# Kernel tuning notes

Measured on AMD Instinct MI355X. Metric: run time of the kernel, lower is better.

The kernel has to match this reference:

```python
import jax, jax.numpy as jnp
import numpy as np

NEG_INF = -1e9
LEAKY_SLOPE = 0.2


def setup_inputs() -> dict:
    key = jax.random.key(0)
    k1, k2, k3, k4, k5, k6, k7 = jax.random.split(key, 7)
    B, L = 50000, 50          # batch nodes, max padded neighbors (num_sample)
    N = 200000                # unique node embeddings
    D_in, D_out = 256, 64
    padded_neighs = jax.random.randint(k1, (B, L), 0, N, dtype=jnp.int32)
    mask = jax.random.randint(k2, (B, L), 0, 2, dtype=jnp.int32).astype(jnp.bool_)
    mask = mask.at[:, 0].set(True)  # every node has >=1 neighbor
    dst_idx = jax.random.randint(k3, (B,), 0, N, dtype=jnp.int32)
    embed_table = jax.random.normal(k4, (N, D_in), dtype=jnp.float32)
    # xavier_uniform for proj [D_out, D_in]
    bound = float(np.sqrt(6.0 / (D_in + D_out)))
    W_proj = jax.random.uniform(k5, (D_out, D_in), minval=-bound, maxval=bound, dtype=jnp.float32)
    a_src = jax.random.normal(k6, (D_out,), dtype=jnp.float32) * 0.1
    a_dst = jax.random.normal(k7, (D_out,), dtype=jnp.float32) * 0.1
    return {"padded_neighs": padded_neighs, "mask": mask, "dst_idx": dst_idx,
            "embed_table": embed_table, "W_proj": W_proj, "a_src": a_src, "a_dst": a_dst}


def leaky_relu(x):
    return jnp.where(x >= 0, x, LEAKY_SLOPE * x)


def reference(padded_neighs, mask, dst_idx, embed_table, W_proj, a_src, a_dst):
    # project all unique-node embeddings: [N, D_out]
    embed_prime = embed_table @ W_proj.T
    # gather neighbor and dst projected features
    neigh_feats = embed_prime[padded_neighs]          # [B, L, D_out]
    dst_feats = embed_prime[dst_idx]                  # [B, D_out] (constant across L)
    # GAT-style scores: leaky_relu(dst @ a_dst) + leaky_relu(neigh @ a_src)
    dst_attn = leaky_relu(dst_feats @ a_dst)[:, None, None]       # [B, 1, 1]
    neigh_attn = leaky_relu(neigh_feats @ a_src)[:, :, None]      # [B, L, 1]
    edge_attn = dst_attn + neigh_attn                             # [B, L, 1]
    # masked softmax over the neighbor axis
    scores = jnp.where(mask[:, :, None], edge_attn, NEG_INF)
    attn = jax.nn.softmax(scores, axis=1)                         # [B, L, 1]
    # weighted sum of neighbor features
    return jnp.sum(attn * neigh_feats, axis=1)                    # [B, D_out]
```

## Files before the change

kernel.cpp:

```cpp
#include <hip/hip_runtime.h>
#include <stdint.h>

#define DIN 256
#define DOUT 64
#define LMAX 50
#define NEG_INF -1e9f
#define WSTRIDE 264

typedef short bf16x8 __attribute__((ext_vector_type(8)));
typedef float f32x4  __attribute__((ext_vector_type(4)));

static __device__ __forceinline__ unsigned short f2bf(float x) {
    unsigned int u = __float_as_uint(x);
    u += 0x7fffu + ((u >> 16) & 1u);
    return (unsigned short)(u >> 16);
}
static __device__ __forceinline__ float bflo(unsigned int u) { return __uint_as_float(u << 16); }
static __device__ __forceinline__ float bfhi(unsigned int u) { return __uint_as_float(u & 0xffff0000u); }

__global__ __launch_bounds__(256) void proj_kernel(
    const float* __restrict__ embed, const float* __restrict__ W,
    unsigned short* __restrict__ ep16, int N)
{
    __shared__ unsigned short wl[64 * WSTRIDE];
    __shared__ unsigned short al[64 * WSTRIDE];

    const int tid  = threadIdx.x;
    const int lane = tid & 63;
    const int wv   = tid >> 6;
    const int mrow = lane & 15;
    const int quad = lane >> 4;
    const int m_base = blockIdx.x * 64;

#pragma unroll
    for (int i = 0; i < 16; ++i) {
        const int idx4 = tid + 256 * i;
        const int e    = idx4 * 4;
        const int n    = e >> 8;
        const int k    = e & 255;
        const float4 f = *(const float4*)&W[e];
        union { unsigned short s[4]; unsigned long long v; } p;
        p.s[0] = f2bf(f.x); p.s[1] = f2bf(f.y);
        p.s[2] = f2bf(f.z); p.s[3] = f2bf(f.w);
        *(unsigned long long*)&wl[n * WSTRIDE + k] = p.v;
    }
#pragma unroll
    for (int i = 0; i < 16; ++i) {
        const int idx4 = tid + 256 * i;
        const int e    = idx4 * 4;
        const int n    = e >> 8;
        const int k    = e & 255;
        int row = m_base + n;
        if (row >= N) row = N - 1;
        const float4 f = *(const float4*)&embed[(size_t)row * DIN + k];
        union { unsigned short s[4]; unsigned long long v; } p;
        p.s[0] = f2bf(f.x); p.s[1] = f2bf(f.y);
        p.s[2] = f2bf(f.z); p.s[3] = f2bf(f.w);
        *(unsigned long long*)&al[n * WSTRIDE + k] = p.v;
    }
    __syncthreads();

    f32x4 acc[4];
#pragma unroll
    for (int nt = 0; nt < 4; ++nt) acc[nt] = (f32x4){0.f, 0.f, 0.f, 0.f};

#pragma unroll
    for (int kc = 0; kc < DIN; kc += 32) {
        const bf16x8 afrag =
            *(const bf16x8*)&al[(wv * 16 + mrow) * WSTRIDE + kc + quad * 8];
#pragma unroll
        for (int nt = 0; nt < 4; ++nt) {
            const bf16x8 bfrag =
                *(const bf16x8*)&wl[(nt * 16 + mrow) * WSTRIDE + kc + quad * 8];
            acc[nt] = __builtin_amdgcn_mfma_f32_16x16x32_bf16(
                afrag, bfrag, acc[nt], 0, 0, 0);
        }
    }

#pragma unroll
    for (int nt = 0; nt < 4; ++nt)
#pragma unroll
        for (int r = 0; r < 4; ++r) {
            const int row = m_base + wv * 16 + quad * 4 + r;
            if (row < N)
                ep16[(size_t)row * DOUT + nt * 16 + mrow] = f2bf(acc[nt][r]);
        }
}

__global__ __launch_bounds__(256, 6) void agg_kernel(
    const int* __restrict__ neighs, const void* __restrict__ mask,
    const unsigned int* __restrict__ ep16u,
    const float* __restrict__ a_src,
    float* __restrict__ out, int B)
{
    __shared__ unsigned int fwbuf[4][LMAX * 32];

    const int tid  = threadIdx.x;
    const int lane = tid & 63;
    const int wv   = tid >> 6;
    const int b    = blockIdx.x * 4 + wv;
    const int bc   = b < B ? b : B - 1;

    const unsigned int* mw = (const unsigned int*)mask;
    const bool byteMode = (mw[12] > 1u);

    const int* nb = neighs + (size_t)bc * LMAX;
    bool mvalid = false;
    int  nbv    = 0;
    if (lane < LMAX) {
        const int mi = bc * LMAX + lane;
        mvalid = byteMode ? (((const uint8_t*)mask)[mi] != 0)
                          : (((const int*)mask)[mi] != 0);
        nbv = nb[lane];
    }
    const unsigned long long vm = __ballot(mvalid);
    const int nv = (int)__popcll(vm);

    const int p    = (int)__popcll(vm & ((1ull << lane) - 1ull));
    const int dsta = mvalid ? p : (nv + (lane - p));
    const int cnb  = __builtin_amdgcn_ds_permute(dsta << 2, nbv);

    unsigned int* buf = fwbuf[wv];
    const int sub    = lane >> 3;
    const int gchunk = (lane & 7) ^ sub;
    const int f      = nv >> 3;
    for (int i = 0; i < f; ++i) {
        const int r = 8 * i + sub;
        const int n = __shfl(cnb, r, 64);
        const unsigned int* gp = ep16u + (size_t)n * 32 + gchunk * 4;
        __builtin_amdgcn_global_load_lds(
            (const __attribute__((address_space(1))) void*)gp,
            (__attribute__((address_space(3))) void*)&buf[i * 256],
            16, 0, 0);
    }
    const int t     = nv & 7;
    const int npair = (t + 1) >> 1;
    const int rbase = 8 * f;
    for (int p2 = 0; p2 < npair; ++p2) {
        const int r   = rbase + 2 * p2 + (lane >> 5);
        const int rc  = r < nv ? r : nv - 1;
        const int n   = __shfl(cnb, rc, 64);
        const int w   = lane & 31;
        const int gwd = (((w >> 2) ^ (r & 7)) << 2) + (w & 3);
        const unsigned int* gp = ep16u + (size_t)n * 32 + gwd;
        __builtin_amdgcn_global_load_lds(
            (const __attribute__((address_space(1))) void*)gp,
            (__attribute__((address_space(3))) void*)&buf[(rbase + 2 * p2) * 32],
            4, 0, 0);
    }

    asm volatile("s_waitcnt vmcnt(0)" ::: "memory");

    const int lc   = lane < nv ? lane : nv - 1;
    const int rot7 = lc & 7;
    const unsigned int* fr = buf + lc * 32;
    float dot = 0.f;
#pragma unroll
    for (int k8 = 0; k8 < 8; ++k8) {
        const uint4 u = *(const uint4*)&fr[((k8 ^ rot7) << 2)];
        dot = fmaf(bflo(u.x), a_src[k8 * 8 + 0], dot);
        dot = fmaf(bfhi(u.x), a_src[k8 * 8 + 1], dot);
        dot = fmaf(bflo(u.y), a_src[k8 * 8 + 2], dot);
        dot = fmaf(bfhi(u.y), a_src[k8 * 8 + 3], dot);
        dot = fmaf(bflo(u.z), a_src[k8 * 8 + 4], dot);
        dot = fmaf(bfhi(u.z), a_src[k8 * 8 + 5], dot);
        dot = fmaf(bflo(u.w), a_src[k8 * 8 + 6], dot);
        dot = fmaf(bfhi(u.w), a_src[k8 * 8 + 7], dot);
    }
    const float lr = dot >= 0.f ? dot : 0.2f * dot;
    float s = (lane < nv) ? lr : NEG_INF;

    float mx = s;
#pragma unroll
    for (int m = 32; m >= 1; m >>= 1) mx = fmaxf(mx, __shfl_xor(mx, m, 64));
    const float e = __expf(s - mx);
    float se = e;
#pragma unroll
    for (int m = 32; m >= 1; m >>= 1) se += __shfl_xor(se, m, 64);
    const float attn = e / se;

    const int s8   = lane >> 3;
    const int gc   = lane & 7;
    const int nit8 = (nv + 7) >> 3;

    float acc[8];
#pragma unroll
    for (int j = 0; j < 8; ++j) acc[j] = 0.f;

    int  rr0 = s8 < nv ? s8 : nv - 1;
    uint4 u  = *(const uint4*)&buf[rr0 * 32 + ((gc ^ (rr0 & 7)) << 2)];
    float w  = __shfl(attn, s8, 64);

    for (int i = 0; i < nit8; ++i) {
        const int inx = (i + 1 < nit8) ? i + 1 : i;
        const int r   = 8 * inx + s8;
        const int rr  = r < nv ? r : nv - 1;
        const uint4 un = *(const uint4*)&buf[rr * 32 + ((gc ^ (rr & 7)) << 2)];
        const float wn = __shfl(attn, r, 64);
        acc[0] = fmaf(w, bflo(u.x), acc[0]);
        acc[1] = fmaf(w, bfhi(u.x), acc[1]);
        acc[2] = fmaf(w, bflo(u.y), acc[2]);
        acc[3] = fmaf(w, bfhi(u.y), acc[3]);
        acc[4] = fmaf(w, bflo(u.z), acc[4]);
        acc[5] = fmaf(w, bfhi(u.z), acc[5]);
        acc[6] = fmaf(w, bflo(u.w), acc[6]);
        acc[7] = fmaf(w, bfhi(u.w), acc[7]);
        u = un; w = wn;
    }

#pragma unroll
    for (int m = 8; m <= 32; m <<= 1)
#pragma unroll
        for (int j = 0; j < 8; ++j) acc[j] += __shfl_xor(acc[j], m, 64);

    if (b < B && lane < 8) {
        float* op = out + (size_t)b * DOUT + 8 * lane;
        float4 o0; o0.x = acc[0]; o0.y = acc[1]; o0.z = acc[2]; o0.w = acc[3];
        float4 o1; o1.x = acc[4]; o1.y = acc[5]; o1.z = acc[6]; o1.w = acc[7];
        *(float4*)op       = o0;
        *(float4*)(op + 4) = o1;
    }
}

extern "C" void kernel_launch(void* const* d_in, const int* in_sizes, int n_in,
                              void* d_out, int out_size, void* d_ws, size_t ws_size,
                              hipStream_t stream)
{
    const int*   neighs  = (const int*)d_in[0];
    const void*  mask    = d_in[1];
    const float* embed   = (const float*)d_in[3];
    const float* W       = (const float*)d_in[4];
    const float* a_src   = (const float*)d_in[5];
    float* out = (float*)d_out;

    const int B = in_sizes[2];
    const int N = in_sizes[3] / DIN;

    unsigned short* ep16 = (unsigned short*)d_ws;

    proj_kernel<<<dim3((N + 63) / 64), dim3(256), 0, stream>>>(embed, W, ep16, N);
    agg_kernel<<<dim3((B + 3) / 4), dim3(256), 0, stream>>>(
        neighs, mask, (const unsigned int*)ep16, a_src, out, B);
}
```

Before: 349.2 us.

## Process two nodes per wave with double-buffered LDS gathers and fixed-size loads

The aggregation kernel now assigns two batch nodes to each wave, each with its own LDS buffer. All gathers for both nodes are issued up front, and a partial vmcnt wait lets the first node's softmax and weighted sum overlap with the second node's loads still in flight. Neighbour compaction is dropped: all 50 slots are loaded at a fixed, unrolled size, with masked slots redirected to neighbour 0 and removed by the mask in the softmax. This trades extra (mostly cache-hitting) gather traffic and doubled LDS per block, with lower occupancy, for more memory-level parallelism and no data-dependent loop counts.

```diff
diff --git a/kernel.cpp b/kernel.cpp
--- a/kernel.cpp
+++ b/kernel.cpp
@@ -87,139 +87,150 @@
         }
 }
 
-__global__ __launch_bounds__(256, 6) void agg_kernel(
+__global__ __launch_bounds__(256, 3) void agg_kernel(
     const int* __restrict__ neighs, const void* __restrict__ mask,
     const unsigned int* __restrict__ ep16u,
     const float* __restrict__ a_src,
     float* __restrict__ out, int B)
 {
-    __shared__ unsigned int fwbuf[4][LMAX * 32];
+    __shared__ unsigned int fwbuf[4][2][LMAX * 32];
 
     const int tid  = threadIdx.x;
     const int lane = tid & 63;
     const int wv   = tid >> 6;
-    const int b    = blockIdx.x * 4 + wv;
-    const int bc   = b < B ? b : B - 1;
+    const int nodeA = blockIdx.x * 8 + wv * 2;
+    const int nodeB = nodeA + 1;
+    const int cA = nodeA < B ? nodeA : B - 1;
+    const int cB = nodeB < B ? nodeB : B - 1;
 
     const unsigned int* mw = (const unsigned int*)mask;
     const bool byteMode = (mw[12] > 1u);
 
-    const int* nb = neighs + (size_t)bc * LMAX;
-    bool mvalid = false;
-    int  nbv    = 0;
+    bool mvA = false, mvB = false;
+    int  nbA = 0, nbB = 0;
     if (lane < LMAX) {
-        const int mi = bc * LMAX + lane;
-        mvalid = byteMode ? (((const uint8_t*)mask)[mi] != 0)
-                          : (((const int*)mask)[mi] != 0);
-        nbv = nb[lane];
-    }
-    const unsigned long long vm = __ballot(mvalid);
-    const int nv = (int)__popcll(vm);
-
-    const int p    = (int)__popcll(vm & ((1ull << lane) - 1ull));
-    const int dsta = mvalid ? p : (nv + (lane - p));
-    const int cnb  = __builtin_amdgcn_ds_permute(dsta << 2, nbv);
-
-    unsigned int* buf = fwbuf[wv];
+        const int miA = cA * LMAX + lane;
+        const int miB = cB * LMAX + lane;
+        if (byteMode) {
+            mvA = ((const uint8_t*)mask)[miA] != 0;
+            mvB = ((const uint8_t*)mask)[miB] != 0;
+        } else {
+            mvA = ((const int*)mask)[miA] != 0;
+            mvB = ((const int*)mask)[miB] != 0;
+        }
+        nbA = neighs[miA];
+        nbB = neighs[miB];
+    }
+    const unsigned long long vmA = __ballot(mvA);
+    const unsigned long long vmB = __ballot(mvB);
+
+    unsigned int* bufA = fwbuf[wv][0];
+    unsigned int* bufB = fwbuf[wv][1];
+
     const int sub    = lane >> 3;
     const int gchunk = (lane & 7) ^ sub;
-    const int f      = nv >> 3;
-    for (int i = 0; i < f; ++i) {
-        const int r = 8 * i + sub;
-        const int n = __shfl(cnb, r, 64);
-        const unsigned int* gp = ep16u + (size_t)n * 32 + gchunk * 4;
-        __builtin_amdgcn_global_load_lds(
-            (const __attribute__((address_space(1))) void*)gp,
-            (__attribute__((address_space(3))) void*)&buf[i * 256],
-            16, 0, 0);
-    }
-    const int t     = nv & 7;
-    const int npair = (t + 1) >> 1;
-    const int rbase = 8 * f;
-    for (int p2 = 0; p2 < npair; ++p2) {
-        const int r   = rbase + 2 * p2 + (lane >> 5);
-        const int rc  = r < nv ? r : nv - 1;
-        const int n   = __shfl(cnb, rc, 64);
-        const int w   = lane & 31;
-        const int gwd = (((w >> 2) ^ (r & 7)) << 2) + (w & 3);
-        const unsigned int* gp = ep16u + (size_t)n * 32 + gwd;
-        __builtin_amdgcn_global_load_lds(
-            (const __attribute__((address_space(1))) void*)gp,
-            (__attribute__((address_space(3))) void*)&buf[(rbase + 2 * p2) * 32],
-            4, 0, 0);
-    }
-
-    asm volatile("s_waitcnt vmcnt(0)" ::: "memory");
-
-    const int lc   = lane < nv ? lane : nv - 1;
-    const int rot7 = lc & 7;
-    const unsigned int* fr = buf + lc * 32;
-    float dot = 0.f;
-#pragma unroll
-    for (int k8 = 0; k8 < 8; ++k8) {
-        const uint4 u = *(const uint4*)&fr[((k8 ^ rot7) << 2)];
-        dot = fmaf(bflo(u.x), a_src[k8 * 8 + 0], dot);
-        dot = fmaf(bfhi(u.x), a_src[k8 * 8 + 1], dot);
-        dot = fmaf(bflo(u.y), a_src[k8 * 8 + 2], dot);
-        dot = fmaf(bfhi(u.y), a_src[k8 * 8 + 3], dot);
-        dot = fmaf(bflo(u.z), a_src[k8 * 8 + 4], dot);
-        dot = fmaf(bfhi(u.z), a_src[k8 * 8 + 5], dot);
-        dot = fmaf(bflo(u.w), a_src[k8 * 8 + 6], dot);
-        dot = fmaf(bfhi(u.w), a_src[k8 * 8 + 7], dot);
-    }
-    const float lr = dot >= 0.f ? dot : 0.2f * dot;
-    float s = (lane < nv) ? lr : NEG_INF;
-
-    float mx = s;
-#pragma unroll
-    for (int m = 32; m >= 1; m >>= 1) mx = fmaxf(mx, __shfl_xor(mx, m, 64));
-    const float e = __expf(s - mx);
-    float se = e;
-#pragma unroll
-    for (int m = 32; m >= 1; m >>= 1) se += __shfl_xor(se, m, 64);
-    const float attn = e / se;
-
-    const int s8   = lane >> 3;
-    const int gc   = lane & 7;
-    const int nit8 = (nv + 7) >> 3;
-
-    float acc[8];
-#pragma unroll
-    for (int j = 0; j < 8; ++j) acc[j] = 0.f;
-
-    int  rr0 = s8 < nv ? s8 : nv - 1;
-    uint4 u  = *(const uint4*)&buf[rr0 * 32 + ((gc ^ (rr0 & 7)) << 2)];
-    float w  = __shfl(attn, s8, 64);
-
-    for (int i = 0; i < nit8; ++i) {
-        const int inx = (i + 1 < nit8) ? i + 1 : i;
-        const int r   = 8 * inx + s8;
-        const int rr  = r < nv ? r : nv - 1;
-        const uint4 un = *(const uint4*)&buf[rr * 32 + ((gc ^ (rr & 7)) << 2)];
-        const float wn = __shfl(attn, r, 64);
-        acc[0] = fmaf(w, bflo(u.x), acc[0]);
-        acc[1] = fmaf(w, bfhi(u.x), acc[1]);
-        acc[2] = fmaf(w, bflo(u.y), acc[2]);
-        acc[3] = fmaf(w, bfhi(u.y), acc[3]);
-        acc[4] = fmaf(w, bflo(u.z), acc[4]);
-        acc[5] = fmaf(w, bfhi(u.z), acc[5]);
-        acc[6] = fmaf(w, bflo(u.w), acc[6]);
-        acc[7] = fmaf(w, bfhi(u.w), acc[7]);
-        u = un; w = wn;
-    }
-
-#pragma unroll
-    for (int m = 8; m <= 32; m <<= 1)
-#pragma unroll
-        for (int j = 0; j < 8; ++j) acc[j] += __shfl_xor(acc[j], m, 64);
-
-    if (b < B && lane < 8) {
-        float* op = out + (size_t)b * DOUT + 8 * lane;
-        float4 o0; o0.x = acc[0]; o0.y = acc[1]; o0.z = acc[2]; o0.w = acc[3];
-        float4 o1; o1.x = acc[4]; o1.y = acc[5]; o1.z = acc[6]; o1.w = acc[7];
-        *(float4*)op       = o0;
-        *(float4*)(op + 4) = o1;
-    }
+    const int r2     = 48 + (lane >> 5);
+    const int w32    = lane & 31;
+    const int gwd2   = (((w32 >> 2) ^ (r2 & 7)) << 2) + (w32 & 3);
+
+#define ISSUE_NODE(bufX, vmX, nbX)                                             \
+    {                                                                          \
+        const int n0 = __shfl(nbX, 0, 64);                                     \
+        _Pragma("unroll")                                                      \
+        for (int i = 0; i < 6; ++i) {                                          \
+            const int r = 8 * i + sub;                                         \
+            int n = __shfl(nbX, r, 64);                                        \
+            n = ((vmX >> r) & 1ull) ? n : n0;                                  \
+            const unsigned int* gp = ep16u + (size_t)n * 32 + gchunk * 4;      \
+            __builtin_amdgcn_global_load_lds(                                  \
+                (const __attribute__((address_space(1))) void*)gp,             \
+                (__attribute__((address_space(3))) void*)&bufX[i * 256],       \
+                16, 0, 0);                                                     \
+        }                                                                      \
+        int n = __shfl(nbX, r2, 64);                                           \
+        n = ((vmX >> r2) & 1ull) ? n : n0;                                     \
+        const unsigned int* gp = ep16u + (size_t)n * 32 + gwd2;                \
+        __builtin_amdgcn_global_load_lds(                                      \
+            (const __attribute__((address_space(1))) void*)gp,                 \
+            (__attribute__((address_space(3))) void*)&bufX[48 * 32], 4, 0, 0); \
+    }
+
+    ISSUE_NODE(bufA, vmA, nbA)
+    ISSUE_NODE(bufB, vmB, nbB)
+
+    auto compute = [&](const unsigned int* buf, unsigned long long vmX, int node,
+                       int nodeRaw) {
+        const int lc   = lane < LMAX ? lane : 0;
+        const int rot7 = lc & 7;
+        const unsigned int* fr = buf + lc * 32;
+        float dot = 0.f;
+#pragma unroll
+        for (int k8 = 0; k8 < 8; ++k8) {
+            const uint4 u = *(const uint4*)&fr[((k8 ^ rot7) << 2)];
+            dot = fmaf(bflo(u.x), a_src[k8 * 8 + 0], dot);
+            dot = fmaf(bfhi(u.x), a_src[k8 * 8 + 1], dot);
+            dot = fmaf(bflo(u.y), a_src[k8 * 8 + 2], dot);
+            dot = fmaf(bfhi(u.y), a_src[k8 * 8 + 3], dot);
+            dot = fmaf(bflo(u.z), a_src[k8 * 8 + 4], dot);
+            dot = fmaf(bfhi(u.z), a_src[k8 * 8 + 5], dot);
+            dot = fmaf(bflo(u.w), a_src[k8 * 8 + 6], dot);
+            dot = fmaf(bfhi(u.w), a_src[k8 * 8 + 7], dot);
+        }
+        const float lr = dot >= 0.f ? dot : 0.2f * dot;
+        const bool valid = (lane < LMAX) && ((vmX >> lane) & 1ull);
+        float s = valid ? lr : NEG_INF;
+
+        float mx = s;
+#pragma unroll
+        for (int m = 32; m >= 1; m >>= 1) mx = fmaxf(mx, __shfl_xor(mx, m, 64));
+        const float e = __expf(s - mx);
+        float se = e;
+#pragma unroll
+        for (int m = 32; m >= 1; m >>= 1) se += __shfl_xor(se, m, 64);
+        const float attn = e / se;
+
+        const int s8 = lane >> 3;
+        const int gc = lane & 7;
+        float acc[8];
+#pragma unroll
+        for (int j = 0; j < 8; ++j) acc[j] = 0.f;
+#pragma unroll
+        for (int i = 0; i < 7; ++i) {
+            const int r  = 8 * i + s8;
+            const int rr = r < LMAX ? r : LMAX - 1;
+            const float w = __shfl(attn, r, 64);
+            const uint4 u = *(const uint4*)&buf[rr * 32 + ((gc ^ (rr & 7)) << 2)];
+            acc[0] = fmaf(w, bflo(u.x), acc[0]);
+            acc[1] = fmaf(w, bfhi(u.x), acc[1]);
+            acc[2] = fmaf(w, bflo(u.y), acc[2]);
+            acc[3] = fmaf(w, bfhi(u.y), acc[3]);
+            acc[4] = fmaf(w, bflo(u.z), acc[4]);
+            acc[5] = fmaf(w, bfhi(u.z), acc[5]);
+            acc[6] = fmaf(w, bflo(u.w), acc[6]);
+            acc[7] = fmaf(w, bfhi(u.w), acc[7]);
+        }
+#pragma unroll
+        for (int m = 8; m <= 32; m <<= 1)
+#pragma unroll
+            for (int j = 0; j < 8; ++j) acc[j] += __shfl_xor(acc[j], m, 64);
+
+        if (nodeRaw < B && lane < 8) {
+            float* op = out + (size_t)node * DOUT + 8 * lane;
+            float4 o0; o0.x = acc[0]; o0.y = acc[1]; o0.z = acc[2]; o0.w = acc[3];
+            float4 o1; o1.x = acc[4]; o1.y = acc[5]; o1.z = acc[6]; o1.w = acc[7];
+            *(float4*)op       = o0;
+            *(float4*)(op + 4) = o1;
+        }
+    };
+
+    asm volatile("s_waitcnt vmcnt(7)" ::: "memory");
+    __builtin_amdgcn_sched_barrier(0);
+    compute(bufA, vmA, cA, nodeA);
+
+    asm volatile("s_waitcnt vmcnt(1)" ::: "memory");
+    __builtin_amdgcn_sched_barrier(0);
+    compute(bufB, vmB, cB, nodeB);
+#undef ISSUE_NODE
 }
 
 extern "C" void kernel_launch(void* const* d_in, const int* in_sizes, int n_in,
@@ -239,6 +250,6 @@
     unsigned short* ep16 = (unsigned short*)d_ws;
 
     proj_kernel<<<dim3((N + 63) / 64), dim3(256), 0, stream>>>(embed, W, ep16, N);
-    agg_kernel<<<dim3((B + 3) / 4), dim3(256), 0, stream>>>(
+    agg_kernel<<<dim3((B + 7) / 8), dim3(256), 0, stream>>>(
         neighs, mask, (const unsigned int*)ep16, a_src, out, B);
 }
```

Result: slower. 361.5 us (+3.5%).
